# Kernel optimization log

Measured on AMD Instinct MI355X. Metric: run time of the kernel, lower is better.

Reference implementation:

```python
import jax, jax.numpy as jnp
import numpy as np


def setup_inputs() -> dict:
    key = jax.random.key(0)
    k1, k2, k3, k4 = jax.random.split(key, 4)
    B, C, H, W = 4, 64, 128, 256
    Cout, kH, kW = 64, 3, 3
    x = jax.random.normal(k1, (B, C, H, W), dtype=jnp.float32)
    # offset layout: channel 2*(i*kW+j) = dy, 2*(i*kW+j)+1 = dx (deformable_groups=1)
    offset = jax.random.normal(k2, (B, 2 * kH * kW, H, W), dtype=jnp.float32)
    weight = jax.random.normal(k3, (Cout, C, kH, kW), dtype=jnp.float32) * 0.05
    bias = jax.random.normal(k4, (Cout,), dtype=jnp.float32) * 0.05
    return {"x": x, "offset": offset, "weight": weight, "bias": bias}


STRIDE, PAD, DIL = 1, 1, 1


def _deform_conv(x, offset, weight, bias):
    B, C, H, W = x.shape
    Cout, Cin, kH, kW = weight.shape
    K = kH * kW
    Ho = (H + 2 * PAD - DIL * (kH - 1) - 1) // STRIDE + 1
    Wo = (W + 2 * PAD - DIL * (kW - 1) - 1) // STRIDE + 1

    hs = (jnp.arange(Ho) * STRIDE - PAD).astype(jnp.float32)  # [Ho]
    ws = (jnp.arange(Wo) * STRIDE - PAD).astype(jnp.float32)  # [Wo]
    ki, kj = jnp.meshgrid(jnp.arange(kH), jnp.arange(kW), indexing="ij")
    ki = (ki.reshape(K) * DIL).astype(jnp.float32)  # [K]
    kj = (kj.reshape(K) * DIL).astype(jnp.float32)

    off = offset.reshape(B, K, 2, Ho, Wo)
    dy, dx = off[:, :, 0], off[:, :, 1]  # [B,K,Ho,Wo]
    py = hs[None, None, :, None] + ki[None, :, None, None] + dy  # [B,K,Ho,Wo]
    px = ws[None, None, None, :] + kj[None, :, None, None] + dx

    y0 = jnp.floor(py)
    x0 = jnp.floor(px)
    ly = py - y0
    lx = px - x0
    y0i = y0.astype(jnp.int32)
    x0i = x0.astype(jnp.int32)

    def gather(xb, yi, xi):
        # xb: [C,H,W]; yi, xi: [K,Ho,Wo]; zero for out-of-bounds corners
        valid = (yi >= 0) & (yi < H) & (xi >= 0) & (xi < W)
        yc = jnp.clip(yi, 0, H - 1)
        xc = jnp.clip(xi, 0, W - 1)
        idx = (yc * W + xc).reshape(-1)
        g = jnp.take(xb.reshape(C, H * W), idx, axis=1).reshape(C, K, Ho, Wo)
        return g * valid[None].astype(xb.dtype)

    gather_b = jax.vmap(gather)
    corners = [
        (y0i, x0i, (1.0 - ly) * (1.0 - lx)),
        (y0i, x0i + 1, (1.0 - ly) * lx),
        (y0i + 1, x0i, ly * (1.0 - lx)),
        (y0i + 1, x0i + 1, ly * lx),
    ]
    vals = jnp.zeros((B, C, K, Ho, Wo), dtype=x.dtype)
    for yi, xi, w in corners:
        vals = vals + gather_b(x, yi, xi) * w[:, None]  # broadcast over C

    out = jnp.einsum("bckhw,ock->bohw", vals, weight.reshape(Cout, Cin, K))
    return out + bias[None, :, None, None]


def reference(x, offset, weight, bias):
    return _deform_conv(x, offset, weight, bias)
```

## Files before the change

kernel.cpp:

```cpp
#include <hip/hip_runtime.h>

typedef float floatx4 __attribute__((ext_vector_type(4)));
typedef _Float16 half2v __attribute__((ext_vector_type(2)));
typedef _Float16 half8 __attribute__((ext_vector_type(8)));

#define Hh 128
#define Ww 256
#define Cc 64
#define COUT 64
#define Bb 4
#define HW (Hh*Ww)
#define VP 74

__global__ void prep(const float* __restrict__ x, const float* __restrict__ wsrc,
                     _Float16* __restrict__ xn, unsigned short* __restrict__ wdst) {
    const int bx = blockIdx.x, h = blockIdx.y, b = blockIdx.z;
    const int tid = threadIdx.x;
    if (bx == 2) {
        const int i = (h + Hh * b) * 72 + tid;
        if (tid < 72) {
            const int kt = i % 9, c = (i / 9) % Cc, o = i / (9 * Cc);
            _Float16 hv = (_Float16)wsrc[i];
            wdst[(kt * COUT + o) * Cc + c] = *(unsigned short*)&hv;
        }
        return;
    }
    __shared__ unsigned short T[128][VP];
    const int wl = tid & 127;
    const int ch = tid >> 7;
    const float* sp = x + ((b * Cc + ch * 32) * Hh + h) * Ww + bx * 128 + wl;
    float vb[32];
#pragma unroll
    for (int c = 0; c < 32; ++c) vb[c] = sp[c * HW];
#pragma unroll
    for (int c2 = 0; c2 < 16; ++c2) {
        half2v hv; hv.x = (_Float16)vb[2 * c2]; hv.y = (_Float16)vb[2 * c2 + 1];
        *(unsigned*)&T[wl][ch * 32 + 2 * c2] = *(unsigned*)&hv;
    }
    __syncthreads();
    uint4* drow = (uint4*)(xn + ((size_t)(b * Hh + h) * Ww + bx * 128) * 64);
#pragma unroll
    for (int j = 0; j < 4; ++j) {
        const int idx = j * 256 + tid;
        drow[idx] = *(const uint4*)&T[idx >> 3][(idx & 7) * 8];
    }
}

__device__ __forceinline__ void lds_barrier() {
    asm volatile("s_waitcnt lgkmcnt(0)\n\ts_barrier" ::: "memory");
}

struct Tap {
    half2v W00, W01, W10, W11;
    int a00, a01, a10, a11;
};

template<int I>
__device__ __forceinline__ unsigned (&sel3(unsigned (&a)[16], unsigned (&b)[16],
                                           unsigned (&c)[16]))[16] {
    if constexpr (I == 0) return a; else if constexpr (I == 1) return b; else return c;
}
template<int I>
__device__ __forceinline__ Tap& sel3t(Tap& a, Tap& b, Tap& c) {
    if constexpr (I == 0) return a; else if constexpr (I == 1) return b; else return c;
}

__device__ __forceinline__ void tap_setup(int kt, int h, int w, float dy, float dx,
                                          int cg, Tap& t) {
    const int ki = kt / 3, kj = kt % 3;
    const float py = (float)(h - 1 + ki) + dy;
    const float px = (float)(w - 1 + kj) + dx;
    const float y0f = floorf(py), x0f = floorf(px);
    const int y0 = (int)y0f, x0 = (int)x0f;
    const float ly = py - y0f, lx = px - x0f;
    const int y1 = y0 + 1, x1 = x0 + 1;
    const bool vy0 = ((unsigned)y0 < Hh), vy1 = ((unsigned)y1 < Hh);
    const bool vx0 = ((unsigned)x0 < Ww), vx1 = ((unsigned)x1 < Ww);
    const float w00 = (vy0 && vx0) ? (1.f - ly) * (1.f - lx) : 0.f;
    const float w01 = (vy0 && vx1) ? (1.f - ly) * lx : 0.f;
    const float w10 = (vy1 && vx0) ? ly * (1.f - lx) : 0.f;
    const float w11 = (vy1 && vx1) ? ly * lx : 0.f;
    _Float16 h00 = (_Float16)w00, h01 = (_Float16)w01;
    _Float16 h10 = (_Float16)w10, h11 = (_Float16)w11;
    t.W00.x = h00; t.W00.y = h00;  t.W01.x = h01; t.W01.y = h01;
    t.W10.x = h10; t.W10.y = h10;  t.W11.x = h11; t.W11.y = h11;
    const int y0c = min(max(y0, 0), Hh - 1), y1c = min(max(y1, 0), Hh - 1);
    const int x0c = min(max(x0, 0), Ww - 1), x1c = min(max(x1, 0), Ww - 1);
    t.a00 = (y0c * Ww + x0c) * 8 + cg;
    t.a01 = (y0c * Ww + x1c) * 8 + cg;
    t.a10 = (y1c * Ww + x0c) * 8 + cg;
    t.a11 = (y1c * Ww + x1c) * 8 + cg;
}

__device__ __forceinline__ void tap_load(const uint4* __restrict__ xb4, const Tap& t,
                                         unsigned (&pf)[16]) {
    *(uint4*)&pf[0]  = xb4[t.a00];
    *(uint4*)&pf[4]  = xb4[t.a01];
    *(uint4*)&pf[8]  = xb4[t.a10];
    *(uint4*)&pf[12] = xb4[t.a11];
}

__device__ __forceinline__ void wf_load(const unsigned short* __restrict__ wt,
                                        half8 (&WF)[4]) {
    WF[0] = *(const half8*)(wt);
    WF[1] = *(const half8*)(wt + 16 * Cc);
    WF[2] = *(const half8*)(wt + 32);
    WF[3] = *(const half8*)(wt + 16 * Cc + 32);
}

__device__ __forceinline__ void tap_store(const Tap& t, const unsigned (&pf)[16],
                                          unsigned short* __restrict__ vrow) {
    unsigned o[4];
#pragma unroll
    for (int s = 0; s < 4; ++s) {
        half2v v = (*(const half2v*)&pf[s])      * t.W00
                 + (*(const half2v*)&pf[4 + s])  * t.W01
                 + (*(const half2v*)&pf[8 + s])  * t.W10
                 + (*(const half2v*)&pf[12 + s]) * t.W11;
        o[s] = *(unsigned*)&v;
    }
    uint4 u; u.x = o[0]; u.y = o[1]; u.z = o[2]; u.w = o[3];
    *(uint4*)vrow = u;
}

__device__ __forceinline__ void mfma_tap(const half8 (&WF)[4],
                                         const unsigned short* __restrict__ Vbuf,
                                         int nt, int ln, floatx4 (&acc)[2]) {
#pragma unroll
    for (int g = 0; g < 2; ++g) {
        const int pp = nt * 16 + (ln & 15);
        half8 bfrag = *(const half8*)&Vbuf[pp * VP + g * 32 + (ln >> 4) * 8];
        acc[0] = __builtin_amdgcn_mfma_f32_16x16x32_f16(WF[2 * g],     bfrag, acc[0], 0, 0, 0);
        acc[1] = __builtin_amdgcn_mfma_f32_16x16x32_f16(WF[2 * g + 1], bfrag, acc[1], 0, 0, 0);
    }
}

template<int KT>
__device__ __forceinline__ void pipe_iter(
    const uint4* __restrict__ xb4, const float* __restrict__ offb,
    const unsigned short* __restrict__ wfb,
    const unsigned short* __restrict__ V0, const unsigned short* __restrict__ V1,
    unsigned short* __restrict__ vrow0, unsigned short* __restrict__ vrow1,
    int h, int w, int cg, int nt, int ln,
    Tap& tpA, Tap& tpB, Tap& tpC,
    unsigned (&pfA)[16], unsigned (&pfB)[16], unsigned (&pfC)[16],
    half8 (&WF0)[4], half8 (&WF1)[4],
    float& dy0, float& dx0, float& dy1, float& dx1,
    floatx4 (&acc)[2])
{
    constexpr int S = KT & 1;
    wf_load(wfb + KT * COUT * Cc, S ? WF1 : WF0);
    if constexpr (KT + 2 <= 8) {
        constexpr int GI = (KT + 2) % 3;
        Tap& tg = sel3t<GI>(tpA, tpB, tpC);
        tap_setup(KT + 2, h, w, S ? dy1 : dy0, S ? dx1 : dx0, cg, tg);
        tap_load(xb4, tg, sel3<GI>(pfA, pfB, pfC));
    }
    if constexpr (KT + 4 <= 8) {
        (S ? dy1 : dy0) = offb[(2 * (KT + 4)) * HW];
        (S ? dx1 : dx0) = offb[(2 * (KT + 4) + 1) * HW];
    }
    constexpr int Tm = 1 - S;
    mfma_tap(Tm ? WF1 : WF0, Tm ? V1 : V0, nt, ln, acc);
    constexpr int SI = KT % 3;
    tap_store(sel3t<SI>(tpA, tpB, tpC), sel3<SI>(pfA, pfB, pfC),
              S ? vrow1 : vrow0);
    lds_barrier();
}

__launch_bounds__(256, 4)
__global__ void dcn_mfma(const _Float16* __restrict__ xn,
                         const float* __restrict__ offset,
                         const unsigned short* __restrict__ wb,
                         const float* __restrict__ bias,
                         float* __restrict__ out) {
    __shared__ unsigned short V[2][32 * VP];

    const int tid = threadIdx.x;
    const int p   = tid >> 3;
    const int cg  = tid & 7;
    const int wv  = tid >> 6;
    const int ln  = tid & 63;

    const int b  = blockIdx.z;
    const int h  = blockIdx.y;
    const int w0 = blockIdx.x * 32;
    const int w  = w0 + p;

    const uint4* xb4  = (const uint4*)(xn + (size_t)b * HW * 64);
    const float* offb = offset + b * 18 * HW + h * Ww + w;
    unsigned short* vrow0 = &V[0][p * VP + cg * 8];
    unsigned short* vrow1 = &V[1][p * VP + cg * 8];

    const int nt = wv & 1;
    const int mb = (wv >> 1) * 2;
    const unsigned short* wfb = wb + (mb * 16 + (ln & 15)) * Cc + (ln >> 4) * 8;

    floatx4 acc[2];
    acc[0] = (floatx4)0.f; acc[1] = (floatx4)0.f;

    unsigned pfA[16], pfB[16], pfC[16];
    half8 WF0[4], WF1[4];
    Tap tpA, tpB, tpC;

    float dy0 = offb[0],        dx0 = offb[HW];
    float dy1 = offb[2 * HW],   dx1 = offb[3 * HW];
    wf_load(wfb, WF0);
    tap_setup(0, h, w, dy0, dx0, cg, tpA);
    tap_load(xb4, tpA, pfA);
    tap_setup(1, h, w, dy1, dx1, cg, tpB);
    tap_load(xb4, tpB, pfB);
    dy0 = offb[4 * HW]; dx0 = offb[5 * HW];
    dy1 = offb[6 * HW]; dx1 = offb[7 * HW];
    tap_setup(2, h, w, dy0, dx0, cg, tpC);
    tap_load(xb4, tpC, pfC);
    dy0 = offb[8 * HW]; dx0 = offb[9 * HW];
    tap_store(tpA, pfA, vrow0);
    lds_barrier();

#define PI(K) pipe_iter<K>(xb4, offb, wfb, V[0], V[1], vrow0, vrow1, h, w, cg, nt, ln, \
                           tpA, tpB, tpC, pfA, pfB, pfC, WF0, WF1,                     \
                           dy0, dx0, dy1, dx1, acc)
    PI(1); PI(2); PI(3); PI(4); PI(5); PI(6); PI(7); PI(8);
#undef PI

    mfma_tap(WF0, V[0], nt, ln, acc);

    float* outp = out + b * COUT * HW + h * Ww;
    const int col = w0 + nt * 16 + (ln & 15);
#pragma unroll
    for (int mi = 0; mi < 2; ++mi)
#pragma unroll
        for (int r = 0; r < 4; ++r) {
            const int o = (mb + mi) * 16 + (ln >> 4) * 4 + r;
            outp[o * HW + col] = acc[mi][r] + bias[o];
        }
}

extern "C" void kernel_launch(void* const* d_in, const int* in_sizes, int n_in,
                              void* d_out, int out_size, void* d_ws, size_t ws_size,
                              hipStream_t stream) {
    const float* x      = (const float*)d_in[0];
    const float* offset = (const float*)d_in[1];
    const float* weight = (const float*)d_in[2];
    const float* bias   = (const float*)d_in[3];
    float* out = (float*)d_out;

    _Float16* xn = (_Float16*)d_ws;
    unsigned short* wb = (unsigned short*)((char*)d_ws + (size_t)Bb * HW * Cc * 2);

    prep<<<dim3(3, Hh, Bb), 256, 0, stream>>>(x, weight, xn, wb);
    dcn_mfma<<<dim3(Ww / 32, Hh, Bb), 256, 0, stream>>>(xn, offset, wb, bias, out);
}
```

Baseline: 178.3 us.

## Restructure prep transpose and pre-swizzle weights into MFMA fragment order

The prep kernel is rebuilt around 512-thread blocks that each cover 8 channels by 8 rows of x. Each block reads x with float4 loads into a float LDS tile, then writes 8-channel fp16 chunks into the NHWC buffer. The weight conversion now stores weights in the exact per-lane MFMA fragment order, so each wave's weight loads in the main kernel become contiguous 16-byte reads at lane*8. The trade-off is that the large LDS tile limits prep occupancy, and the NHWC writes are now strided by 128 bytes per lane instead of fully contiguous.

```diff
diff --git a/kernel.cpp b/kernel.cpp
--- a/kernel.cpp
+++ b/kernel.cpp
@@ -12,37 +12,52 @@
 #define HW (Hh*Ww)
 #define VP 74
 
+__launch_bounds__(512, 4)
 __global__ void prep(const float* __restrict__ x, const float* __restrict__ wsrc,
                      _Float16* __restrict__ xn, unsigned short* __restrict__ wdst) {
-    const int bx = blockIdx.x, h = blockIdx.y, b = blockIdx.z;
+    const int bid = blockIdx.x;
     const int tid = threadIdx.x;
-    if (bx == 2) {
-        const int i = (h + Hh * b) * 72 + tid;
+    if (bid >= 512) {
+        const int i = (bid - 512) * 72 + tid;
         if (tid < 72) {
             const int kt = i % 9, c = (i / 9) % Cc, o = i / (9 * Cc);
+            const int mbh = o >> 5, mi = (o >> 4) & 1, r = o & 15;
+            const int g = c >> 5, ks = (c >> 3) & 3, s = c & 7;
+            const int ln = ks * 16 + r, j = g * 2 + mi;
             _Float16 hv = (_Float16)wsrc[i];
-            wdst[(kt * COUT + o) * Cc + c] = *(unsigned short*)&hv;
+            wdst[(((kt * 2 + mbh) * 4 + j) * 64 + ln) * 8 + s] = *(unsigned short*)&hv;
         }
         return;
     }
-    __shared__ unsigned short T[128][VP];
-    const int wl = tid & 127;
-    const int ch = tid >> 7;
-    const float* sp = x + ((b * Cc + ch * 32) * Hh + h) * Ww + bx * 128 + wl;
-    float vb[32];
-#pragma unroll
-    for (int c = 0; c < 32; ++c) vb[c] = sp[c * HW];
-#pragma unroll
-    for (int c2 = 0; c2 < 16; ++c2) {
-        half2v hv; hv.x = (_Float16)vb[2 * c2]; hv.y = (_Float16)vb[2 * c2 + 1];
-        *(unsigned*)&T[wl][ch * 32 + 2 * c2] = *(unsigned*)&hv;
+    const int cg = bid >> 6;
+    const int T  = bid & 63;
+    const int b  = T >> 4;
+    const int ht = T & 15;
+    __shared__ float Tf[64][260];
+    const float* src = x + ((size_t)(b * Cc + cg * 8) * Hh + ht * 8) * Ww;
+#pragma unroll
+    for (int s = 0; s < 8; ++s) {
+        const int u   = s * 512 + tid;
+        const int row = u >> 6;
+        const int wq  = u & 63;
+        const float4 v = *(const float4*)(src + (size_t)(row >> 3) * HW + (row & 7) * Ww + wq * 4);
+        *(float4*)&Tf[row][wq * 4] = v;
     }
     __syncthreads();
-    uint4* drow = (uint4*)(xn + ((size_t)(b * Hh + h) * Ww + bx * 128) * 64);
-#pragma unroll
-    for (int j = 0; j < 4; ++j) {
-        const int idx = j * 256 + tid;
-        drow[idx] = *(const uint4*)&T[idx >> 3][(idx & 7) * 8];
+#pragma unroll
+    for (int j2 = 0; j2 < 4; ++j2) {
+        const int idx = j2 * 512 + tid;
+        const int hh = idx >> 8, w = idx & 255;
+        unsigned o4[4];
+#pragma unroll
+        for (int cp = 0; cp < 4; ++cp) {
+            half2v hv;
+            hv.x = (_Float16)Tf[(2 * cp) * 8 + hh][w];
+            hv.y = (_Float16)Tf[(2 * cp + 1) * 8 + hh][w];
+            o4[cp] = *(unsigned*)&hv;
+        }
+        uint4 u4; u4.x = o4[0]; u4.y = o4[1]; u4.z = o4[2]; u4.w = o4[3];
+        *(uint4*)(xn + ((size_t)(b * Hh + ht * 8 + hh) * Ww + w) * 64 + cg * 8) = u4;
     }
 }
 
@@ -103,9 +118,9 @@
 __device__ __forceinline__ void wf_load(const unsigned short* __restrict__ wt,
                                         half8 (&WF)[4]) {
     WF[0] = *(const half8*)(wt);
-    WF[1] = *(const half8*)(wt + 16 * Cc);
-    WF[2] = *(const half8*)(wt + 32);
-    WF[3] = *(const half8*)(wt + 16 * Cc + 32);
+    WF[1] = *(const half8*)(wt + 512);
+    WF[2] = *(const half8*)(wt + 1024);
+    WF[3] = *(const half8*)(wt + 1536);
 }
 
 __device__ __forceinline__ void tap_store(const Tap& t, const unsigned (&pf)[16],
@@ -149,7 +164,7 @@
     floatx4 (&acc)[2])
 {
     constexpr int S = KT & 1;
-    wf_load(wfb + KT * COUT * Cc, S ? WF1 : WF0);
+    wf_load(wfb + KT * 4096, S ? WF1 : WF0);
     if constexpr (KT + 2 <= 8) {
         constexpr int GI = (KT + 2) % 3;
         Tap& tg = sel3t<GI>(tpA, tpB, tpC);
@@ -194,7 +209,7 @@
 
     const int nt = wv & 1;
     const int mb = (wv >> 1) * 2;
-    const unsigned short* wfb = wb + (mb * 16 + (ln & 15)) * Cc + (ln >> 4) * 8;
+    const unsigned short* wfb = wb + (wv >> 1) * 2048 + ln * 8;
 
     floatx4 acc[2];
     acc[0] = (floatx4)0.f; acc[1] = (floatx4)0.f;
@@ -249,6 +264,6 @@
     _Float16* xn = (_Float16*)d_ws;
     unsigned short* wb = (unsigned short*)((char*)d_ws + (size_t)Bb * HW * Cc * 2);
 
-    prep<<<dim3(3, Hh, Bb), 256, 0, stream>>>(x, weight, xn, wb);
+    prep<<<dim3(1024), 512, 0, stream>>>(x, weight, xn, wb);
     dcn_mfma<<<dim3(Ww / 32, Hh, Bb), 256, 0, stream>>>(xn, offset, wb, bias, out);
 }
```

Result: faster. 143.7 us, median of 2 (-19.4%).
